# Kernel tuning notes

Measured on AMD Instinct MI355X. Metric: run time of the kernel, lower is better.

## Reference

```python
import jax, jax.numpy as jnp
import numpy as np

N = 100000   # active voxels
K = 27       # 3x3x3 kernel offsets
C = 64       # in_channels == out_channels (residual block)
EPS = 1e-5


def setup_inputs() -> dict:
    key = jax.random.key(0)
    ks = jax.random.split(key, 10)
    feats = jax.random.normal(ks[0], (N, C), dtype=jnp.float32)
    # kernel-map: for each voxel, index of the neighbor voxel for each of the 27 offsets
    nbr = jax.random.randint(ks[1], (N, K), 0, N)
    nbr = nbr.at[:, K // 2].set(jnp.arange(N))  # center offset is identity
    w_scale = 1.0 / np.sqrt(K * C)
    W1 = jax.random.normal(ks[2], (K, C, C), dtype=jnp.float32) * w_scale
    b1 = jax.random.normal(ks[3], (C,), dtype=jnp.float32) * 0.01
    g1 = jnp.ones((C,), jnp.float32)
    be1 = jnp.zeros((C,), jnp.float32)
    W2 = jax.random.normal(ks[4], (K, C, C), dtype=jnp.float32) * w_scale
    b2 = jax.random.normal(ks[5], (C,), dtype=jnp.float32) * 0.01
    g2 = jnp.ones((C,), jnp.float32)
    be2 = jnp.zeros((C,), jnp.float32)
    return {"feats": feats, "nbr": nbr, "W1": W1, "b1": b1, "g1": g1, "be1": be1,
            "W2": W2, "b2": b2, "g2": g2, "be2": be2}


def _sparse_conv(f, nbr, W, b):
    # gather neighbor features per kernel offset: [N, K, C]
    g = f[nbr]
    # per-offset matmul and reduce over offsets (gather-matmul-scatter form)
    return jnp.einsum('nkc,kcd->nd', g, W) + b


def _bn(x, gamma, beta):
    # BatchNorm over active voxels (training-mode batch stats, per channel)
    mu = x.mean(axis=0)
    var = x.var(axis=0)
    return (x - mu) * jax.lax.rsqrt(var + EPS) * gamma + beta


def reference(feats, nbr, W1, b1, g1, be1, W2, b2, g2, be2):
    h = jax.nn.relu(_bn(_sparse_conv(feats, nbr, W1, b1), g1, be1))
    h = _bn(_sparse_conv(h, nbr, W2, b2), g2, be2)
    return jax.nn.relu(h + feats)  # residual add + ReLU
```

## Files before the change

### kernel.cpp

```cpp
#include <hip/hip_runtime.h>

#define NCH 64
#define KOFF 27
#define EPSV 1e-5f

typedef __attribute__((ext_vector_type(8))) short  bf16x8;
typedef __attribute__((ext_vector_type(4))) float  f32x4;
typedef __attribute__((ext_vector_type(8))) unsigned short u16x8;

__device__ __forceinline__ unsigned short f2bf(float x) {
    unsigned int u = __float_as_uint(x);
    u += 0x7fffu + ((u >> 16) & 1u);
    return (unsigned short)(u >> 16);
}

__global__ __launch_bounds__(256)
void prep_kernel(const float* __restrict__ feats,
                 const float* __restrict__ W1, const float* __restrict__ W2,
                 unsigned short* __restrict__ fbf,
                 unsigned short* __restrict__ wt1, unsigned short* __restrict__ wt2,
                 float* __restrict__ stat, int total8)
{
    const int b = blockIdx.x;
    if (b == 0) {
        stat[threadIdx.x] = 0.f;
        return;
    }
    if (b <= 108) {
        const float* W = (b <= 54) ? W1 : W2;
        unsigned short* Wt = (b <= 54) ? wt1 : wt2;
        const int t = (b <= 54 ? b - 1 : b - 55) * 256 + threadIdx.x;
        const int l  = t & 63;
        const int ct = (t >> 6) & 3;
        const int s  = (t >> 8) & 1;
        const int k  = t >> 9;
        const int d     = ct * 16 + (l & 15);
        const int cbase = s * 32 + (l >> 4) * 8;
        u16x8 o;
#pragma unroll
        for (int j = 0; j < 8; ++j)
            o[j] = f2bf(W[(size_t)k * 4096 + (size_t)(cbase + j) * 64 + d]);
        reinterpret_cast<u16x8*>(Wt)[t] = o;
        return;
    }
    const int idx = (b - 109) * 256 + threadIdx.x;
    if (idx >= total8) return;
    const float4* xp = reinterpret_cast<const float4*>(feats) + (size_t)idx * 2;
    const float4 a = xp[0], c = xp[1];
    u16x8 o;
    o[0] = f2bf(a.x); o[1] = f2bf(a.y); o[2] = f2bf(a.z); o[3] = f2bf(a.w);
    o[4] = f2bf(c.x); o[5] = f2bf(c.y); o[6] = f2bf(c.z); o[7] = f2bf(c.w);
    reinterpret_cast<u16x8*>(fbf)[idx] = o;
}

__global__ __launch_bounds__(256, 4)
void conv_mfma_kernel(const unsigned short* __restrict__ fin,
                      const int* __restrict__ nbr,
                      const unsigned short* __restrict__ Wt,
                      const float* __restrict__ bias,
                      float* __restrict__ out, float* __restrict__ pstat, int N)
{
    __shared__ int            s_idx[128 * KOFF];
    __shared__ unsigned short s_w[3 * 4096];

    const int lane = threadIdx.x & 63;
    const int wv   = threadIdx.x >> 6;
    const int n0   = blockIdx.x * 128;
    const int m    = lane & 15;
    const int quad = lane >> 4;

    {
        const int rem  = N - n0;
        const int maxi = (rem < 128 ? rem : 128) * KOFF;
        const int* nb  = nbr + (size_t)n0 * KOFF;
        for (int p = threadIdx.x; p < 128 * KOFF; p += 256)
            s_idx[p] = ((p < maxi) ? nb[p] : 0) * (NCH * 2);
    }
    __syncthreads();

    f32x4 acc[2][4];
#pragma unroll
    for (int mt = 0; mt < 2; ++mt)
#pragma unroll
        for (int ct = 0; ct < 4; ++ct) acc[mt][ct] = (f32x4){0.f, 0.f, 0.f, 0.f};

    bf16x8 A[2][2][2];
    bf16x8 B[2][4];
    const char* finB = (const char*)fin;
    const int lv0 = wv * 32;

#define LOADA(kk)                                                            \
    {                                                                        \
        _Pragma("unroll")                                                    \
        for (int mt = 0; mt < 2; ++mt) {                                     \
            const int ofs = s_idx[(lv0 + mt * 16 + m) * KOFF + (kk)];        \
            const char* fp = finB + ofs + quad * 16;                         \
            A[(kk) & 1][mt][0] = *reinterpret_cast<const bf16x8*>(fp);       \
            A[(kk) & 1][mt][1] = *reinterpret_cast<const bf16x8*>(fp + 64);  \
        }                                                                    \
    }

#define LOADB_LDS(kk)                                                        \
    {                                                                        \
        const unsigned short* wp = s_w + (kk) * 4096 + lane * 8;             \
        _Pragma("unroll")                                                    \
        for (int s = 0; s < 2; ++s)                                          \
            _Pragma("unroll")                                                \
            for (int ct = 0; ct < 4; ++ct)                                   \
                B[s][ct] =                                                   \
                    *reinterpret_cast<const bf16x8*>(wp + (s * 4 + ct) * 512);\
    }

#define DOMFMA(kk)                                                           \
    {                                                                        \
        _Pragma("unroll")                                                    \
        for (int mt = 0; mt < 2; ++mt)                                       \
            _Pragma("unroll")                                                \
            for (int s = 0; s < 2; ++s)                                      \
                _Pragma("unroll")                                            \
                for (int ct = 0; ct < 4; ++ct)                               \
                    acc[mt][ct] = __builtin_amdgcn_mfma_f32_16x16x32_bf16(   \
                        A[(kk) & 1][mt][s], B[s][ct], acc[mt][ct], 0, 0, 0); \
    }

    LOADA(0);

#pragma unroll
    for (int c = 0; c < 9; ++c) {
        const int kb = c * 3;

        {
            const u16x8* gw = reinterpret_cast<const u16x8*>(
                Wt + (size_t)kb * 4096);
            u16x8* lw = reinterpret_cast<u16x8*>(s_w);
#pragma unroll
            for (int i = 0; i < 6; ++i)
                lw[threadIdx.x + i * 256] = gw[threadIdx.x + i * 256];
        }
        __syncthreads();

        LOADA(kb + 1);
        LOADB_LDS(0);
        __builtin_amdgcn_sched_barrier(0);
        DOMFMA(kb);

        LOADA(kb + 2);
        LOADB_LDS(1);
        __builtin_amdgcn_sched_barrier(0);
        DOMFMA(kb + 1);

        if (c < 8) LOADA(kb + 3);
        LOADB_LDS(2);
        __builtin_amdgcn_sched_barrier(0);
        DOMFMA(kb + 2);

        __syncthreads();
    }
#undef LOADA
#undef LOADB_LDS
#undef DOMFMA

#pragma unroll
    for (int ct = 0; ct < 4; ++ct) {
        const int ch = ct * 16 + m;
        const float bv = bias[ch];
        float s = 0.f, q = 0.f;
#pragma unroll
        for (int mt = 0; mt < 2; ++mt) {
#pragma unroll
            for (int r = 0; r < 4; ++r) {
                const int vox = n0 + lv0 + mt * 16 + quad * 4 + r;
                if (vox < N) {
                    const float v = acc[mt][ct][r] + bv;
                    out[(size_t)vox * NCH + ch] = v;
                    s += v;
                    q += v * v;
                }
            }
        }
        s += __shfl_xor(s, 16, 64);
        s += __shfl_xor(s, 32, 64);
        q += __shfl_xor(q, 16, 64);
        q += __shfl_xor(q, 32, 64);
        if (quad == 0) {
            float* pr = pstat + ((size_t)blockIdx.x * 4 + wv) * 128;
            pr[ch]      = s;
            pr[64 + ch] = q;
        }
    }
}

__global__ __launch_bounds__(256)
void reduce_stats_kernel(const float* __restrict__ pstat, float* __restrict__ stat,
                         int rows)
{
    __shared__ float s_[256];
    const int ch = threadIdx.x & 127;
    const int h  = threadIdx.x >> 7;
    float acc = 0.f;
    for (int r = blockIdx.x * 2 + h; r < rows; r += gridDim.x * 2)
        acc += pstat[(size_t)r * 128 + ch];
    s_[threadIdx.x] = acc;
    __syncthreads();
    if (threadIdx.x < 128)
        atomicAdd(&stat[threadIdx.x], s_[threadIdx.x] + s_[threadIdx.x + 128]);
}

__global__ __launch_bounds__(256)
void bn_relu_bf16_kernel(const float* __restrict__ x, const float* __restrict__ sums,
                         const float* __restrict__ gmm, const float* __restrict__ bet,
                         float invN, unsigned short* __restrict__ y, int total8)
{
    const int idx = blockIdx.x * 256 + threadIdx.x;
    if (idx >= total8) return;
    const int c0 = (idx & 7) * 8;
    const float4* xp = reinterpret_cast<const float4*>(x) + (size_t)idx * 2;
    const float4 a = xp[0], b = xp[1];
    float v[8] = {a.x, a.y, a.z, a.w, b.x, b.y, b.z, b.w};
    u16x8 o;
#pragma unroll
    for (int i = 0; i < 8; ++i) {
        const int c = c0 + i;
        const float mu  = sums[c] * invN;
        const float var = sums[64 + c] * invN - mu * mu;
        const float rs  = rsqrtf(var + EPSV);
        const float sc  = gmm[c] * rs;
        const float sh  = bet[c] - mu * sc;
        o[i] = f2bf(fmaxf(fmaf(v[i], sc, sh), 0.f));
    }
    reinterpret_cast<u16x8*>(y)[idx] = o;
}

__global__ __launch_bounds__(256)
void bn_res_relu_kernel(float* __restrict__ x, const float* __restrict__ feats,
                        const float* __restrict__ sums, const float* __restrict__ gmm,
                        const float* __restrict__ bet, float invN, int total4)
{
    const int idx = blockIdx.x * blockDim.x + threadIdx.x;
    if (idx >= total4) return;
    float4 v = reinterpret_cast<float4*>(x)[idx];
    const float4 f = reinterpret_cast<const float4*>(feats)[idx];
    const int c0 = (idx & 15) * 4;
    float sc[4], sh[4];
#pragma unroll
    for (int i = 0; i < 4; ++i) {
        const int c = c0 + i;
        const float mu  = sums[c] * invN;
        const float var = sums[64 + c] * invN - mu * mu;
        const float rs  = rsqrtf(var + EPSV);
        sc[i] = gmm[c] * rs;
        sh[i] = bet[c] - mu * sc[i];
    }
    v.x = fmaxf(fmaf(v.x, sc[0], sh[0]) + f.x, 0.f);
    v.y = fmaxf(fmaf(v.y, sc[1], sh[1]) + f.y, 0.f);
    v.z = fmaxf(fmaf(v.z, sc[2], sh[2]) + f.z, 0.f);
    v.w = fmaxf(fmaf(v.w, sc[3], sh[3]) + f.w, 0.f);
    reinterpret_cast<float4*>(x)[idx] = v;
}

extern "C" void kernel_launch(void* const* d_in, const int* in_sizes, int n_in,
                              void* d_out, int out_size, void* d_ws, size_t ws_size,
                              hipStream_t stream)
{
    const float* feats = (const float*)d_in[0];
    const int*   nbr   = (const int*)d_in[1];
    const float* W1    = (const float*)d_in[2];
    const float* b1    = (const float*)d_in[3];
    const float* g1    = (const float*)d_in[4];
    const float* be1   = (const float*)d_in[5];
    const float* W2    = (const float*)d_in[6];
    const float* b2    = (const float*)d_in[7];
    const float* g2    = (const float*)d_in[8];
    const float* be2   = (const float*)d_in[9];
    float* out = (float*)d_out;

    const int N  = in_sizes[0] / NCH;
    const int NC = N * NCH;
    const float invN = 1.0f / (float)N;

    float*          h0   = (float*)d_ws;
    unsigned short* fbf  = (unsigned short*)(h0 + NC);
    unsigned short* hbf  = fbf + NC;
    unsigned short* wt1  = hbf + NC;
    unsigned short* wt2  = wt1 + KOFF * 4096;
    float*          stat = (float*)(wt2 + KOFF * 4096);

    const int total8   = NC / 8;
    const int castGrid = (total8 + 255) / 256;
    const int prepGrid = 1 + 108 + castGrid;
    const int convGrid = (N + 127) / 128;
    const int statRows = convGrid * 4;

    float* pstat1 = out;
    float* pstat2 = h0;

    prep_kernel<<<prepGrid, 256, 0, stream>>>(feats, W1, W2, fbf, wt1, wt2,
                                              stat, total8);
    conv_mfma_kernel<<<convGrid, 256, 0, stream>>>(fbf, nbr, wt1, b1, h0,
                                                   pstat1, N);
    reduce_stats_kernel<<<32, 256, 0, stream>>>(pstat1, stat, statRows);
    bn_relu_bf16_kernel<<<castGrid, 256, 0, stream>>>(h0, stat, g1, be1, invN,
                                                      hbf, total8);
    conv_mfma_kernel<<<convGrid, 256, 0, stream>>>(hbf, nbr, wt2, b2, out,
                                                   pstat2, N);
    reduce_stats_kernel<<<32, 256, 0, stream>>>(pstat2, stat + 128, statRows);
    bn_res_relu_kernel<<<(NC / 4 + 255) / 256, 256, 0, stream>>>(
        out, feats, stat + 128, g2, be2, invN, NC / 4);
}
```

Measured before the change: 286.3 us.

## Fuse BN stats and apply into conv via grid barrier, keep accumulators in registers

Each conv kernel now reduces its per-channel sums in LDS and atomically adds them to global stats. It then waits at a software grid-wide barrier and applies BN (plus ReLU, or residual+ReLU) directly from the register accumulators. This drops the fp32 intermediate write/read and the separate reduce and BN kernels. Weight staging shrinks to two offsets per iteration, freeing LDS, and the offset loop is no longer unrolled. The grid barrier needs all 782 blocks to be co-resident, which the 4-blocks-per-CU launch bound is meant to allow on 256 CUs. Otherwise it could deadlock, and spinning blocks hold resources while they wait.

```diff
diff --git a/kernel.cpp b/kernel.cpp
--- a/kernel.cpp
+++ b/kernel.cpp
@@ -12,6 +12,20 @@
     unsigned int u = __float_as_uint(x);
     u += 0x7fffu + ((u >> 16) & 1u);
     return (unsigned short)(u >> 16);
+}
+
+__device__ __forceinline__ void grid_arrive_wait(unsigned* bar, unsigned nblk)
+{
+    __syncthreads();
+    if (threadIdx.x == 0) {
+        __threadfence();
+        __hip_atomic_fetch_add(bar, 1u, __ATOMIC_ACQ_REL,
+                               __HIP_MEMORY_SCOPE_AGENT);
+        while (__hip_atomic_load(bar, __ATOMIC_ACQUIRE,
+                                 __HIP_MEMORY_SCOPE_AGENT) < nblk)
+            __builtin_amdgcn_s_sleep(16);
+    }
+    __syncthreads();
 }
 
 __global__ __launch_bounds__(256)
@@ -24,6 +38,8 @@
     const int b = blockIdx.x;
     if (b == 0) {
         stat[threadIdx.x] = 0.f;
+        if (threadIdx.x < 2)
+            ((unsigned*)(stat + 256))[threadIdx.x] = 0u;
         return;
     }
     if (b <= 108) {
@@ -54,14 +70,18 @@
 }
 
 __global__ __launch_bounds__(256, 4)
-void conv_mfma_kernel(const unsigned short* __restrict__ fin,
-                      const int* __restrict__ nbr,
-                      const unsigned short* __restrict__ Wt,
-                      const float* __restrict__ bias,
-                      float* __restrict__ out, float* __restrict__ pstat, int N)
+void conv_fused(const unsigned short* __restrict__ fin,
+                const int* __restrict__ nbr,
+                const unsigned short* __restrict__ Wt,
+                const float* __restrict__ bias,
+                float* __restrict__ stats,
+                unsigned* __restrict__ bar,
+                const float* __restrict__ gmm, const float* __restrict__ bet,
+                float invN, void* __restrict__ dst,
+                const float* __restrict__ resid, int N, int phase)
 {
     __shared__ int            s_idx[128 * KOFF];
-    __shared__ unsigned short s_w[3 * 4096];
+    __shared__ unsigned short s_w[2 * 4096];
 
     const int lane = threadIdx.x & 63;
     const int wv   = threadIdx.x >> 6;
@@ -89,20 +109,20 @@
     const char* finB = (const char*)fin;
     const int lv0 = wv * 32;
 
-#define LOADA(kk)                                                            \
+#define LOADA(kk, par)                                                       \
     {                                                                        \
         _Pragma("unroll")                                                    \
         for (int mt = 0; mt < 2; ++mt) {                                     \
             const int ofs = s_idx[(lv0 + mt * 16 + m) * KOFF + (kk)];        \
             const char* fp = finB + ofs + quad * 16;                         \
-            A[(kk) & 1][mt][0] = *reinterpret_cast<const bf16x8*>(fp);       \
-            A[(kk) & 1][mt][1] = *reinterpret_cast<const bf16x8*>(fp + 64);  \
+            A[par][mt][0] = *reinterpret_cast<const bf16x8*>(fp);            \
+            A[par][mt][1] = *reinterpret_cast<const bf16x8*>(fp + 64);       \
         }                                                                    \
     }
 
-#define LOADB_LDS(kk)                                                        \
+#define LOADB_LDS(sl)                                                        \
     {                                                                        \
-        const unsigned short* wp = s_w + (kk) * 4096 + lane * 8;             \
+        const unsigned short* wp = s_w + (sl) * 4096 + lane * 8;             \
         _Pragma("unroll")                                                    \
         for (int s = 0; s < 2; ++s)                                          \
             _Pragma("unroll")                                                \
@@ -111,7 +131,7 @@
                     *reinterpret_cast<const bf16x8*>(wp + (s * 4 + ct) * 512);\
     }
 
-#define DOMFMA(kk)                                                           \
+#define DOMFMA(par)                                                          \
     {                                                                        \
         _Pragma("unroll")                                                    \
         for (int mt = 0; mt < 2; ++mt)                                       \
@@ -120,46 +140,51 @@
                 _Pragma("unroll")                                            \
                 for (int ct = 0; ct < 4; ++ct)                               \
                     acc[mt][ct] = __builtin_amdgcn_mfma_f32_16x16x32_bf16(   \
-                        A[(kk) & 1][mt][s], B[s][ct], acc[mt][ct], 0, 0, 0); \
-    }
-
-    LOADA(0);
-
-#pragma unroll
-    for (int c = 0; c < 9; ++c) {
-        const int kb = c * 3;
-
+                        A[par][mt][s], B[s][ct], acc[mt][ct], 0, 0, 0);      \
+    }
+
+    LOADA(0, 0);
+
+#pragma unroll 1
+    for (int kb = 0; kb < KOFF - 1; kb += 2) {
         {
-            const u16x8* gw = reinterpret_cast<const u16x8*>(
-                Wt + (size_t)kb * 4096);
+            const u16x8* gw = reinterpret_cast<const u16x8*>(Wt) + (size_t)kb * 512;
             u16x8* lw = reinterpret_cast<u16x8*>(s_w);
 #pragma unroll
-            for (int i = 0; i < 6; ++i)
+            for (int i = 0; i < 4; ++i)
                 lw[threadIdx.x + i * 256] = gw[threadIdx.x + i * 256];
         }
         __syncthreads();
 
-        LOADA(kb + 1);
+        LOADA(kb + 1, 1);
         LOADB_LDS(0);
         __builtin_amdgcn_sched_barrier(0);
-        DOMFMA(kb);
-
-        LOADA(kb + 2);
+        DOMFMA(0);
+
+        LOADA(kb + 2, 0);
         LOADB_LDS(1);
         __builtin_amdgcn_sched_barrier(0);
-        DOMFMA(kb + 1);
-
-        if (c < 8) LOADA(kb + 3);
-        LOADB_LDS(2);
+        DOMFMA(1);
+
+        __syncthreads();
+    }
+    {
+        const u16x8* gw = reinterpret_cast<const u16x8*>(Wt) + (size_t)26 * 512;
+        u16x8* lw = reinterpret_cast<u16x8*>(s_w);
+#pragma unroll
+        for (int i = 0; i < 2; ++i)
+            lw[threadIdx.x + i * 256] = gw[threadIdx.x + i * 256];
+        __syncthreads();
+        LOADB_LDS(0);
         __builtin_amdgcn_sched_barrier(0);
-        DOMFMA(kb + 2);
-
+        DOMFMA(0);
         __syncthreads();
     }
 #undef LOADA
 #undef LOADB_LDS
 #undef DOMFMA
 
+    float* s_red = reinterpret_cast<float*>(s_w);
 #pragma unroll
     for (int ct = 0; ct < 4; ++ct) {
         const int ch = ct * 16 + m;
@@ -169,10 +194,10 @@
         for (int mt = 0; mt < 2; ++mt) {
 #pragma unroll
             for (int r = 0; r < 4; ++r) {
+                acc[mt][ct][r] += bv;
                 const int vox = n0 + lv0 + mt * 16 + quad * 4 + r;
                 if (vox < N) {
-                    const float v = acc[mt][ct][r] + bv;
-                    out[(size_t)vox * NCH + ch] = v;
+                    const float v = acc[mt][ct][r];
                     s += v;
                     q += v * v;
                 }
@@ -183,79 +208,51 @@
         q += __shfl_xor(q, 16, 64);
         q += __shfl_xor(q, 32, 64);
         if (quad == 0) {
-            float* pr = pstat + ((size_t)blockIdx.x * 4 + wv) * 128;
-            pr[ch]      = s;
-            pr[64 + ch] = q;
+            s_red[wv * 128 + ch]      = s;
+            s_red[wv * 128 + 64 + ch] = q;
         }
     }
-}
-
-__global__ __launch_bounds__(256)
-void reduce_stats_kernel(const float* __restrict__ pstat, float* __restrict__ stat,
-                         int rows)
-{
-    __shared__ float s_[256];
-    const int ch = threadIdx.x & 127;
-    const int h  = threadIdx.x >> 7;
-    float acc = 0.f;
-    for (int r = blockIdx.x * 2 + h; r < rows; r += gridDim.x * 2)
-        acc += pstat[(size_t)r * 128 + ch];
-    s_[threadIdx.x] = acc;
-    __syncthreads();
+    __syncthreads();
+    if (threadIdx.x < 128) {
+        const float v = s_red[threadIdx.x] + s_red[128 + threadIdx.x] +
+                        s_red[256 + threadIdx.x] + s_red[384 + threadIdx.x];
+        atomicAdd(&stats[threadIdx.x], v);
+    }
+
+    grid_arrive_wait(bar, (unsigned)gridDim.x);
+
     if (threadIdx.x < 128)
-        atomicAdd(&stat[threadIdx.x], s_[threadIdx.x] + s_[threadIdx.x + 128]);
-}
-
-__global__ __launch_bounds__(256)
-void bn_relu_bf16_kernel(const float* __restrict__ x, const float* __restrict__ sums,
-                         const float* __restrict__ gmm, const float* __restrict__ bet,
-                         float invN, unsigned short* __restrict__ y, int total8)
-{
-    const int idx = blockIdx.x * 256 + threadIdx.x;
-    if (idx >= total8) return;
-    const int c0 = (idx & 7) * 8;
-    const float4* xp = reinterpret_cast<const float4*>(x) + (size_t)idx * 2;
-    const float4 a = xp[0], b = xp[1];
-    float v[8] = {a.x, a.y, a.z, a.w, b.x, b.y, b.z, b.w};
-    u16x8 o;
-#pragma unroll
-    for (int i = 0; i < 8; ++i) {
-        const int c = c0 + i;
-        const float mu  = sums[c] * invN;
-        const float var = sums[64 + c] * invN - mu * mu;
+        s_red[threadIdx.x] =
+            __hip_atomic_load(&stats[threadIdx.x], __ATOMIC_ACQUIRE,
+                              __HIP_MEMORY_SCOPE_AGENT);
+    __syncthreads();
+
+#pragma unroll
+    for (int ct = 0; ct < 4; ++ct) {
+        const int ch = ct * 16 + m;
+        const float mu  = s_red[ch] * invN;
+        const float var = s_red[64 + ch] * invN - mu * mu;
         const float rs  = rsqrtf(var + EPSV);
-        const float sc  = gmm[c] * rs;
-        const float sh  = bet[c] - mu * sc;
-        o[i] = f2bf(fmaxf(fmaf(v[i], sc, sh), 0.f));
-    }
-    reinterpret_cast<u16x8*>(y)[idx] = o;
-}
-
-__global__ __launch_bounds__(256)
-void bn_res_relu_kernel(float* __restrict__ x, const float* __restrict__ feats,
-                        const float* __restrict__ sums, const float* __restrict__ gmm,
-                        const float* __restrict__ bet, float invN, int total4)
-{
-    const int idx = blockIdx.x * blockDim.x + threadIdx.x;
-    if (idx >= total4) return;
-    float4 v = reinterpret_cast<float4*>(x)[idx];
-    const float4 f = reinterpret_cast<const float4*>(feats)[idx];
-    const int c0 = (idx & 15) * 4;
-    float sc[4], sh[4];
-#pragma unroll
-    for (int i = 0; i < 4; ++i) {
-        const int c = c0 + i;
-        const float mu  = sums[c] * invN;
-        const float var = sums[64 + c] * invN - mu * mu;
-        const float rs  = rsqrtf(var + EPSV);
-        sc[i] = gmm[c] * rs;
-        sh[i] = bet[c] - mu * sc[i];
-    }
-    v.x = fmaxf(fmaf(v.x, sc[0], sh[0]) + f.x, 0.f);
-    v.y = fmaxf(fmaf(v.y, sc[1], sh[1]) + f.y, 0.f);
-    v.z = fmaxf(fmaf(v.z, sc[2], sh[2]) + f.z, 0.f);
-    v.w = fmaxf(fmaf(v.w, sc[3], sh[3]) + f.w, 0.f);
-    reinterpret_cast<float4*>(x)[idx] = v;
+        const float scv = gmm[ch] * rs;
+        const float shv = bet[ch] - mu * scv;
+#pragma unroll
+        for (int mt = 0; mt < 2; ++mt) {
+#pragma unroll
+            for (int r = 0; r < 4; ++r) {
+                const int vox = n0 + lv0 + mt * 16 + quad * 4 + r;
+                if (vox < N) {
+                    const float x = fmaf(acc[mt][ct][r], scv, shv);
+                    if (phase == 0) {
+                        ((unsigned short*)dst)[(size_t)vox * NCH + ch] =
+                            f2bf(fmaxf(x, 0.f));
+                    } else {
+                        ((float*)dst)[(size_t)vox * NCH + ch] =
+                            fmaxf(x + resid[(size_t)vox * NCH + ch], 0.f);
+                    }
+                }
+            }
+        }
+    }
 }
 
 extern "C" void kernel_launch(void* const* d_in, const int* in_sizes, int n_in,
@@ -278,32 +275,26 @@
     const int NC = N * NCH;
     const float invN = 1.0f / (float)N;
 
-    float*          h0   = (float*)d_ws;
-    unsigned short* fbf  = (unsigned short*)(h0 + NC);
+    unsigned short* fbf  = (unsigned short*)d_ws;
     unsigned short* hbf  = fbf + NC;
     unsigned short* wt1  = hbf + NC;
     unsigned short* wt2  = wt1 + KOFF * 4096;
     float*          stat = (float*)(wt2 + KOFF * 4096);
+    unsigned*       bar  = (unsigned*)(stat + 256);
 
     const int total8   = NC / 8;
     const int castGrid = (total8 + 255) / 256;
     const int prepGrid = 1 + 108 + castGrid;
     const int convGrid = (N + 127) / 128;
-    const int statRows = convGrid * 4;
-
-    float* pstat1 = out;
-    float* pstat2 = h0;
 
     prep_kernel<<<prepGrid, 256, 0, stream>>>(feats, W1, W2, fbf, wt1, wt2,
                                               stat, total8);
-    conv_mfma_kernel<<<convGrid, 256, 0, stream>>>(fbf, nbr, wt1, b1, h0,
-                                                   pstat1, N);
-    reduce_stats_kernel<<<32, 256, 0, stream>>>(pstat1, stat, statRows);
-    bn_relu_bf16_kernel<<<castGrid, 256, 0, stream>>>(h0, stat, g1, be1, invN,
-                                                      hbf, total8);
-    conv_mfma_kernel<<<convGrid, 256, 0, stream>>>(hbf, nbr, wt2, b2, out,
-                                                   pstat2, N);
-    reduce_stats_kernel<<<32, 256, 0, stream>>>(pstat2, stat + 128, statRows);
-    bn_res_relu_kernel<<<(NC / 4 + 255) / 256, 256, 0, stream>>>(
-        out, feats, stat + 128, g2, be2, invN, NC / 4);
-}
+
+    conv_fused<<<convGrid, 256, 0, stream>>>(fbf, nbr, wt1, b1, stat, bar,
+                                             g1, be1, invN, (void*)hbf,
+                                             feats, N, 0);
+
+    conv_fused<<<convGrid, 256, 0, stream>>>(hbf, nbr, wt2, b2, stat + 128,
+                                             bar + 1, g2, be2, invN,
+                                             (void*)out, feats, N, 1);
+}
```

Result: slower. 720.3 us (+151.6%).

## Fuse BN stat reduction into conv epilogue via padded atomics; store conv1 output as bf16

Applied to the files above, without the earlier changes.

The conv epilogue now reduces per-channel sum and sum-of-squares across its four waves in shared memory, reusing the weight buffer. It then does one atomicAdd per block into a stat array padded to one slot every 16 floats, which removes both reduce_stats launches and the partial-stat round trips. The first conv writes its output as bf16 rather than fp32, halving that tensor's write and re-read traffic. The cost is atomic contention across roughly 780 blocks, a small extra rounding of pre-BN activations, and the BN statistics for conv1 are computed from the unrounded values.

```diff
diff --git a/kernel.cpp b/kernel.cpp
--- a/kernel.cpp
+++ b/kernel.cpp
@@ -13,6 +13,7 @@
     u += 0x7fffu + ((u >> 16) & 1u);
     return (unsigned short)(u >> 16);
 }
+
 
 __global__ __launch_bounds__(256)
 void prep_kernel(const float* __restrict__ feats,
@@ -23,7 +24,9 @@
 {
     const int b = blockIdx.x;
     if (b == 0) {
-        stat[threadIdx.x] = 0.f;
+#pragma unroll
+        for (int i = 0; i < 16; ++i)
+            stat[threadIdx.x + i * 256] = 0.f;
         return;
     }
     if (b <= 108) {
@@ -58,7 +61,8 @@
                       const int* __restrict__ nbr,
                       const unsigned short* __restrict__ Wt,
                       const float* __restrict__ bias,
-                      float* __restrict__ out, float* __restrict__ pstat, int N)
+                      float* __restrict__ statOut,
+                      void* __restrict__ dst, int N, int fp32out)
 {
     __shared__ int            s_idx[128 * KOFF];
     __shared__ unsigned short s_w[3 * 4096];
@@ -160,102 +164,104 @@
 #undef LOADB_LDS
 #undef DOMFMA
 
-#pragma unroll
-    for (int ct = 0; ct < 4; ++ct) {
-        const int ch = ct * 16 + m;
-        const float bv = bias[ch];
-        float s = 0.f, q = 0.f;
-#pragma unroll
-        for (int mt = 0; mt < 2; ++mt) {
-#pragma unroll
-            for (int r = 0; r < 4; ++r) {
-                const int vox = n0 + lv0 + mt * 16 + quad * 4 + r;
-                if (vox < N) {
-                    const float v = acc[mt][ct][r] + bv;
-                    out[(size_t)vox * NCH + ch] = v;
-                    s += v;
-                    q += v * v;
-                }
-            }
-        }
-        s += __shfl_xor(s, 16, 64);
-        s += __shfl_xor(s, 32, 64);
-        q += __shfl_xor(q, 16, 64);
-        q += __shfl_xor(q, 32, 64);
-        if (quad == 0) {
-            float* pr = pstat + ((size_t)blockIdx.x * 4 + wv) * 128;
-            pr[ch]      = s;
-            pr[64 + ch] = q;
-        }
+    float* s_red = reinterpret_cast<float*>(s_w);
+
+#define EPI(STORE_STMT)                                                      \
+    _Pragma("unroll")                                                        \
+    for (int ct = 0; ct < 4; ++ct) {                                         \
+        const int ch = ct * 16 + m;                                          \
+        const float bv = bias[ch];                                           \
+        float s = 0.f, q = 0.f;                                              \
+        _Pragma("unroll")                                                    \
+        for (int mt = 0; mt < 2; ++mt) {                                     \
+            _Pragma("unroll")                                                \
+            for (int r = 0; r < 4; ++r) {                                    \
+                const int vox = n0 + lv0 + mt * 16 + quad * 4 + r;           \
+                if (vox < N) {                                               \
+                    const float v = acc[mt][ct][r] + bv;                     \
+                    STORE_STMT;                                              \
+                    s += v;                                                  \
+                    q += v * v;                                              \
+                }                                                            \
+            }                                                                \
+        }                                                                    \
+        s += __shfl_xor(s, 16, 64);                                          \
+        s += __shfl_xor(s, 32, 64);                                          \
+        q += __shfl_xor(q, 16, 64);                                          \
+        q += __shfl_xor(q, 32, 64);                                          \
+        if (quad == 0) {                                                     \
+            s_red[wv * 128 + ch]      = s;                                   \
+            s_red[wv * 128 + 64 + ch] = q;                                   \
+        }                                                                    \
+    }
+
+    if (fp32out) {
+        EPI(((float*)dst)[(size_t)vox * NCH + ch] = v)
+    } else {
+        EPI(((unsigned short*)dst)[(size_t)vox * NCH + ch] = f2bf(v))
+    }
+#undef EPI
+
+    __syncthreads();
+    if (threadIdx.x < 128) {
+        const float v = s_red[threadIdx.x] + s_red[128 + threadIdx.x] +
+                        s_red[256 + threadIdx.x] + s_red[384 + threadIdx.x];
+        atomicAdd(&statOut[threadIdx.x * 16], v);
     }
 }
 
 __global__ __launch_bounds__(256)
-void reduce_stats_kernel(const float* __restrict__ pstat, float* __restrict__ stat,
-                         int rows)
-{
-    __shared__ float s_[256];
-    const int ch = threadIdx.x & 127;
-    const int h  = threadIdx.x >> 7;
-    float acc = 0.f;
-    for (int r = blockIdx.x * 2 + h; r < rows; r += gridDim.x * 2)
-        acc += pstat[(size_t)r * 128 + ch];
-    s_[threadIdx.x] = acc;
-    __syncthreads();
-    if (threadIdx.x < 128)
-        atomicAdd(&stat[threadIdx.x], s_[threadIdx.x] + s_[threadIdx.x + 128]);
-}
-
-__global__ __launch_bounds__(256)
-void bn_relu_bf16_kernel(const float* __restrict__ x, const float* __restrict__ sums,
+void bn_relu_bf16_kernel(const unsigned short* __restrict__ x,
+                         const float* __restrict__ sums,
                          const float* __restrict__ gmm, const float* __restrict__ bet,
                          float invN, unsigned short* __restrict__ y, int total8)
 {
     const int idx = blockIdx.x * 256 + threadIdx.x;
     if (idx >= total8) return;
     const int c0 = (idx & 7) * 8;
-    const float4* xp = reinterpret_cast<const float4*>(x) + (size_t)idx * 2;
-    const float4 a = xp[0], b = xp[1];
-    float v[8] = {a.x, a.y, a.z, a.w, b.x, b.y, b.z, b.w};
+    const u16x8 v = reinterpret_cast<const u16x8*>(x)[idx];
     u16x8 o;
 #pragma unroll
     for (int i = 0; i < 8; ++i) {
         const int c = c0 + i;
-        const float mu  = sums[c] * invN;
-        const float var = sums[64 + c] * invN - mu * mu;
+        const float mu  = sums[c * 16] * invN;
+        const float var = sums[1024 + c * 16] * invN - mu * mu;
         const float rs  = rsqrtf(var + EPSV);
         const float sc  = gmm[c] * rs;
         const float sh  = bet[c] - mu * sc;
-        o[i] = f2bf(fmaxf(fmaf(v[i], sc, sh), 0.f));
+        const float xv  = __uint_as_float(((unsigned)v[i]) << 16);
+        o[i] = f2bf(fmaxf(fmaf(xv, sc, sh), 0.f));
     }
     reinterpret_cast<u16x8*>(y)[idx] = o;
 }
 
 __global__ __launch_bounds__(256)
-void bn_res_relu_kernel(float* __restrict__ x, const float* __restrict__ feats,
+void bn_res_relu_kernel(const float* __restrict__ x, const float* __restrict__ feats,
                         const float* __restrict__ sums, const float* __restrict__ gmm,
-                        const float* __restrict__ bet, float invN, int total4)
+                        const float* __restrict__ bet, float invN,
+                        float* __restrict__ out, int total4)
 {
     const int idx = blockIdx.x * blockDim.x + threadIdx.x;
     if (idx >= total4) return;
-    float4 v = reinterpret_cast<float4*>(x)[idx];
+    const float4 v = reinterpret_cast<const float4*>(x)[idx];
     const float4 f = reinterpret_cast<const float4*>(feats)[idx];
     const int c0 = (idx & 15) * 4;
     float sc[4], sh[4];
 #pragma unroll
     for (int i = 0; i < 4; ++i) {
         const int c = c0 + i;
-        const float mu  = sums[c] * invN;
-        const float var = sums[64 + c] * invN - mu * mu;
+        const float mu  = sums[c * 16] * invN;
+        const float var = sums[1024 + c * 16] * invN - mu * mu;
         const float rs  = rsqrtf(var + EPSV);
         sc[i] = gmm[c] * rs;
         sh[i] = bet[c] - mu * sc[i];
     }
-    v.x = fmaxf(fmaf(v.x, sc[0], sh[0]) + f.x, 0.f);
-    v.y = fmaxf(fmaf(v.y, sc[1], sh[1]) + f.y, 0.f);
-    v.z = fmaxf(fmaf(v.z, sc[2], sh[2]) + f.z, 0.f);
-    v.w = fmaxf(fmaf(v.w, sc[3], sh[3]) + f.w, 0.f);
-    reinterpret_cast<float4*>(x)[idx] = v;
+    float4 o;
+    o.x = fmaxf(fmaf(v.x, sc[0], sh[0]) + f.x, 0.f);
+    o.y = fmaxf(fmaf(v.y, sc[1], sh[1]) + f.y, 0.f);
+    o.z = fmaxf(fmaf(v.z, sc[2], sh[2]) + f.z, 0.f);
+    o.w = fmaxf(fmaf(v.w, sc[3], sh[3]) + f.w, 0.f);
+    reinterpret_cast<float4*>(out)[idx] = o;
 }
 
 extern "C" void kernel_launch(void* const* d_in, const int* in_sizes, int n_in,
@@ -278,10 +284,11 @@
     const int NC = N * NCH;
     const float invN = 1.0f / (float)N;
 
-    float*          h0   = (float*)d_ws;
-    unsigned short* fbf  = (unsigned short*)(h0 + NC);
-    unsigned short* hbf  = fbf + NC;
-    unsigned short* wt1  = hbf + NC;
+    unsigned short* fbf  = (unsigned short*)d_ws;
+    unsigned short* y1   = fbf + NC;
+    float*          y2   = (float*)d_ws;
+    unsigned short* h1   = y1 + NC;
+    unsigned short* wt1  = h1 + NC;
     unsigned short* wt2  = wt1 + KOFF * 4096;
     float*          stat = (float*)(wt2 + KOFF * 4096);
 
@@ -289,21 +296,19 @@
     const int castGrid = (total8 + 255) / 256;
     const int prepGrid = 1 + 108 + castGrid;
     const int convGrid = (N + 127) / 128;
-    const int statRows = convGrid * 4;
-
-    float* pstat1 = out;
-    float* pstat2 = h0;
 
     prep_kernel<<<prepGrid, 256, 0, stream>>>(feats, W1, W2, fbf, wt1, wt2,
                                               stat, total8);
-    conv_mfma_kernel<<<convGrid, 256, 0, stream>>>(fbf, nbr, wt1, b1, h0,
-                                                   pstat1, N);
-    reduce_stats_kernel<<<32, 256, 0, stream>>>(pstat1, stat, statRows);
-    bn_relu_bf16_kernel<<<castGrid, 256, 0, stream>>>(h0, stat, g1, be1, invN,
-                                                      hbf, total8);
-    conv_mfma_kernel<<<convGrid, 256, 0, stream>>>(hbf, nbr, wt2, b2, out,
-                                                   pstat2, N);
-    reduce_stats_kernel<<<32, 256, 0, stream>>>(pstat2, stat + 128, statRows);
+
+    conv_mfma_kernel<<<convGrid, 256, 0, stream>>>(fbf, nbr, wt1, b1, stat,
+                                                   (void*)y1, N, 0);
+
+    bn_relu_bf16_kernel<<<castGrid, 256, 0, stream>>>(y1, stat, g1, be1, invN,
+                                                      h1, total8);
+
+    conv_mfma_kernel<<<convGrid, 256, 0, stream>>>(h1, nbr, wt2, b2,
+                                                   stat + 2048, (void*)y2, N, 1);
+
     bn_res_relu_kernel<<<(NC / 4 + 255) / 256, 256, 0, stream>>>(
-        out, feats, stat + 128, g2, be2, invN, NC / 4);
-}
+        y2, feats, stat + 2048, g2, be2, invN, out, NC / 4);
+}
```

Result: slower. 299.1 us (+4.5%).
